# Kernel optimization log

Hardware: AMD Instinct MI355X
Metric: run time of the kernel (lower is better)

## Reference

```python
import jax, jax.numpy as jnp
import numpy as np

D_MODEL = 1024
N_HEADS = 16
SEQ = 512  # == max_seq_len; rel-pos bias requires n_token == max_seq_len


def setup_inputs() -> dict:
    key = jax.random.key(0)
    ks = jax.random.split(key, 12)
    B = 16
    x = jax.random.normal(ks[0], (B, SEQ, D_MODEL), dtype=jnp.float32)
    c = jax.random.normal(ks[1], (B, SEQ, 8), dtype=jnp.float32)  # unused by forward
    s = 1.0 / np.sqrt(D_MODEL)
    Wq = jax.random.normal(ks[2], (D_MODEL, D_MODEL), dtype=jnp.float32) * s
    bq = jnp.zeros((D_MODEL,), dtype=jnp.float32)
    Wk = jax.random.normal(ks[3], (D_MODEL, D_MODEL), dtype=jnp.float32) * s
    bk = jnp.zeros((D_MODEL,), dtype=jnp.float32)
    Wv = jax.random.normal(ks[4], (D_MODEL, D_MODEL), dtype=jnp.float32) * s
    bv = jnp.zeros((D_MODEL,), dtype=jnp.float32)
    Wo = jax.random.normal(ks[5], (D_MODEL, D_MODEL), dtype=jnp.float32) * s
    bo = jnp.zeros((D_MODEL,), dtype=jnp.float32)
    # trunc_normal_(std=0.02) approximated by normal*0.02 (values stay small)
    rel_table = jax.random.normal(ks[6], (2 * SEQ - 1, N_HEADS), dtype=jnp.float32) * 0.02
    return {"x": x, "c": c, "Wq": Wq, "bq": bq, "Wk": Wk, "bk": bk,
            "Wv": Wv, "bv": bv, "Wo": Wo, "bo": bo, "rel_table": rel_table}


def reference(x, c, Wq, bq, Wk, bk, Wv, bv, Wo, bo, rel_table):
    # x: [B, S, D]; c is unused in the original forward
    B, S, D = x.shape
    H = N_HEADS
    dk = D // H
    scale = 1.0 / np.sqrt(dk)

    q = (x @ Wq + bq).reshape(B, S, H, dk)
    k = (x @ Wk + bk).reshape(B, S, H, dk)
    v = (x @ Wv + bv).reshape(B, S, H, dk)

    # scores: [B, H, S, S]
    scores = jnp.einsum('bihd,bjhd->bhij', q, k) * scale

    # relative position bias: index[i,j] = i + (S-1-j), values in [0, 2S-2]
    rel_index = jnp.arange(S)[:, None] + jnp.arange(S - 1, -1, -1)[None, :]  # [S,S]
    bias = rel_table[rel_index]            # [S, S, H]
    scores = scores + jnp.transpose(bias, (2, 0, 1))[None]  # [1,H,S,S]

    # causal_mask=False: original adds False * -1e9 == 0, so no mask term
    probs = jax.nn.softmax(scores, axis=-1)

    out = jnp.einsum('bhij,bjhd->bihd', probs, v).reshape(B, S, D)
    return out @ Wo + bo
```

## Files before the change

kernel.cpp:

```cpp
#include <hip/hip_runtime.h>
#include <hip/hip_bf16.h>
#include <stdint.h>

#define D_MODEL 1024
#define NH 16
#define SEQ 512
#define DK 64
#define BATCH 16
#define M_TOT (BATCH*SEQ)

typedef unsigned short u16;
typedef unsigned int u32;
typedef __attribute__((ext_vector_type(8))) __bf16 bf16x8;
typedef __attribute__((ext_vector_type(4))) u16 ushort4v;
typedef __attribute__((ext_vector_type(4))) float f32x4;

static __device__ __forceinline__ u16 f2bf(float f) {
    union { float f; u32 i; } c; c.f = f;
    return (u16)((c.i + 0x8000u) >> 16);
}
static __device__ __forceinline__ u32 cvtpk(float lo, float hi) {
    u32 r; asm("v_cvt_pk_bf16_f32 %0, %1, %2" : "=v"(r) : "v"(lo), "v"(hi)); return r;
}
static __device__ __forceinline__ void async_copy16(const void* g, void* l) {
    __builtin_amdgcn_global_load_lds(
        (const __attribute__((address_space(1))) u32*)g,
        (__attribute__((address_space(3))) u32*)l, 16, 0, 0);
}
static __device__ __forceinline__ float fexp2(float x) {
    float r; asm("v_exp_f32 %0, %1" : "=v"(r) : "v"(x)); return r;
}

__global__ __launch_bounds__(256) void prep(const float* __restrict__ x,
                                            u16* __restrict__ xbf,
                                            const float* __restrict__ Wq,
                                            const float* __restrict__ Wk,
                                            const float* __restrict__ Wv,
                                            u16* __restrict__ Wt3) {
    __shared__ u16 tile[64][65];
    const int bid = blockIdx.x;
    const int t = threadIdx.x;
    if (bid < 2048) {
        #pragma unroll
        for (int it = 0; it < 4; ++it) {
            const int i = (bid * 1024 + it * 256 + t) * 4;
            float4 v = *(const float4*)&x[i];
            ushort4v o;
            o[0] = f2bf(v.x); o[1] = f2bf(v.y); o[2] = f2bf(v.z); o[3] = f2bf(v.w);
            *(ushort4v*)&xbf[i] = o;
        }
        return;
    }
    const int tw = bid - 2048;
    const int z = tw >> 8;
    const float* W = (z == 0) ? Wq : (z == 1) ? Wk : Wv;
    const int n0 = (tw & 15) * 64, k0 = ((tw >> 4) & 15) * 64;
    #pragma unroll
    for (int p = 0; p < 16; ++p) {
        int idx = p * 256 + t;
        int r = idx >> 6, c = idx & 63;
        tile[r][c] = f2bf(W[(size_t)(k0 + r) * D_MODEL + (n0 + c)]);
    }
    __syncthreads();
    #pragma unroll
    for (int p = 0; p < 16; ++p) {
        int idx = p * 256 + t;
        int r = idx >> 6, c = idx & 63;
        Wt3[((size_t)z * D_MODEL + n0 + r) * D_MODEL + (k0 + c)] = tile[c][r];
    }
}

__global__ __launch_bounds__(256) void gemm_bt(const u16* __restrict__ A,
                                               const u16* __restrict__ Bt,
                                               const float* __restrict__ b0,
                                               const float* __restrict__ b1,
                                               const float* __restrict__ b2,
                                               void* __restrict__ o0,
                                               void* __restrict__ o1,
                                               void* __restrict__ o2,
                                               int qkv) {
    __shared__ __attribute__((aligned(16))) u16 smem[16896];
    u16* Asm = smem;
    u16* Bsm = smem + 8192;
    const int t = threadIdx.x;
    const int m0 = blockIdx.y * 128, n0 = blockIdx.x * 128;
    const int lane = t & 63, w = t >> 6;
    const int lm = lane & 15, quad = lane >> 4;
    const int wm = w >> 1, wn = w & 1;

    f32x4 acc[4][4];
    #pragma unroll
    for (int i = 0; i < 4; ++i)
        #pragma unroll
        for (int j = 0; j < 4; ++j) acc[i][j] = (f32x4){0.f, 0.f, 0.f, 0.f};

    for (int kt = 0; kt < D_MODEL / 64; ++kt) {
        const int k0 = kt * 64;
        __syncthreads();
        #pragma unroll
        for (int i = 0; i < 4; ++i) {
            int chunk = i * 256 + t;
            int row = chunk >> 3, c = chunk & 7;
            int cs = c ^ (row & 7);
            async_copy16(A + (size_t)(m0 + row) * D_MODEL + k0 + cs * 8, &Asm[chunk * 8]);
        }
        #pragma unroll
        for (int i = 0; i < 4; ++i) {
            int chunk = i * 256 + t;
            int row = chunk >> 3, c = chunk & 7;
            int cs = c ^ (row & 7);
            async_copy16(Bt + (size_t)(n0 + row) * D_MODEL + k0 + cs * 8, &Bsm[chunk * 8]);
        }
        __syncthreads();
        #pragma unroll
        for (int ks = 0; ks < 64; ks += 32) {
            const int cbase = ks >> 3;
            bf16x8 af[4], bfv[4];
            #pragma unroll
            for (int im = 0; im < 4; ++im) {
                const int row = wm * 64 + im * 16 + lm;
                const int c = (cbase + quad) ^ (row & 7);
                af[im] = *(const bf16x8*)&Asm[row * 64 + c * 8];
            }
            #pragma unroll
            for (int in = 0; in < 4; ++in) {
                const int row = wn * 64 + in * 16 + lm;
                const int c = (cbase + quad) ^ (row & 7);
                bfv[in] = *(const bf16x8*)&Bsm[row * 64 + c * 8];
            }
            #pragma unroll
            for (int im = 0; im < 4; ++im)
                #pragma unroll
                for (int in = 0; in < 4; ++in)
                    acc[im][in] = __builtin_amdgcn_mfma_f32_16x16x32_bf16(
                        af[im], bfv[in], acc[im][in], 0, 0, 0);
        }
    }

    __syncthreads();
    if (qkv) {
        const int sel = n0 >> 10;
        if (sel == 2) {
            #pragma unroll
            for (int in = 0; in < 4; ++in) {
                const int nn = (n0 & 1023) + wn * 64 + in * 16 + lm;
                const float bv = b2[nn];
                const int h = nn >> 6, d = nn & 63;
                #pragma unroll
                for (int im = 0; im < 4; ++im) {
                    const int mb = m0 + wm * 64 + im * 16 + quad * 4;
                    const int b = mb >> 9, s = mb & 511;
                    ushort4v pk;
                    #pragma unroll
                    for (int r = 0; r < 4; ++r) pk[r] = f2bf(acc[im][in][r] + bv);
                    *(ushort4v*)&((u16*)o2)[((size_t)(b * NH + h) * DK + d) * SEQ + s] = pk;
                }
            }
        } else {
            u16* dst = sel ? (u16*)o1 : (u16*)o0;
            const float* bb = sel ? b1 : b0;
            u16 (*Cs)[132] = (u16(*)[132])smem;
            #pragma unroll
            for (int in = 0; in < 4; ++in) {
                const int nl = wn * 64 + in * 16 + lm;
                const float bv = bb[(n0 & 1023) + nl];
                #pragma unroll
                for (int im = 0; im < 4; ++im)
                    #pragma unroll
                    for (int r = 0; r < 4; ++r)
                        Cs[wm * 64 + im * 16 + quad * 4 + r][nl] =
                            f2bf(acc[im][in][r] + bv);
            }
            __syncthreads();
            const int rr = t >> 1, hh = t & 1;
            const int m = m0 + rr;
            const int b = m >> 9, s = m & 511;
            const int h = ((n0 & 1023) >> 6) + hh;
            u16* dp = &dst[((size_t)(b * NH + h) * SEQ + s) * DK];
            #pragma unroll
            for (int c = 0; c < 8; ++c)
                *(uint4*)&dp[c * 8] = *(const uint4*)&Cs[rr][hh * 64 + c * 8];
        }
    } else {
        float (*Cs)[132] = (float(*)[132])smem;
        #pragma unroll
        for (int ph = 0; ph < 2; ++ph) {
            if (wm == ph) {
                #pragma unroll
                for (int in = 0; in < 4; ++in) {
                    const int nl = wn * 64 + in * 16 + lm;
                    const float bv = b0[n0 + nl];
                    #pragma unroll
                    for (int im = 0; im < 4; ++im)
                        #pragma unroll
                        for (int r = 0; r < 4; ++r)
                            Cs[im * 16 + quad * 4 + r][nl] = acc[im][in][r] + bv;
                }
            }
            __syncthreads();
            const int rr = t >> 2, qq = t & 3;
            float* dp = &((float*)o0)[(size_t)(m0 + ph * 64 + rr) * D_MODEL + n0 + qq * 32];
            #pragma unroll
            for (int c = 0; c < 8; ++c)
                *(uint4*)&dp[c * 4] = *(const uint4*)&Cs[rr][qq * 32 + c * 4];
            __syncthreads();
        }
    }
}

__global__ __launch_bounds__(256) void attn_flash(const u16* __restrict__ qg,
                                                  const u16* __restrict__ kg,
                                                  const u16* __restrict__ vTg,
                                                  const float* __restrict__ rel,
                                                  u16* __restrict__ aout,
                                                  const float* __restrict__ Wo,
                                                  u16* __restrict__ WtO) {
    __shared__ __attribute__((aligned(16))) char smem_raw[53760];
    u16* ktb = (u16*)smem_raw;
    u16* vtb = (u16*)(smem_raw + 16384);
    float* biasb = (float*)(smem_raw + 32768);
    u16* qt = (u16*)(smem_raw + 35328);
    u16 (*Pl)[32][72] = (u16(*)[32][72])(smem_raw + 35328);

    const int t = threadIdx.x;
    const int F = blockIdx.x;
    if (F >= 1024) {
        u16 (*tile)[65] = (u16(*)[65])smem_raw;
        const int tw = F - 1024;
        const int n0 = (tw & 15) * 64, k0 = (tw >> 4) * 64;
        #pragma unroll
        for (int p = 0; p < 16; ++p) {
            int idx = p * 256 + t;
            int r = idx >> 6, c = idx & 63;
            tile[r][c] = f2bf(Wo[(size_t)(k0 + r) * D_MODEL + (n0 + c)]);
        }
        __syncthreads();
        #pragma unroll
        for (int p = 0; p < 16; ++p) {
            int idx = p * 256 + t;
            int r = idx >> 6, c = idx & 63;
            WtO[(size_t)(n0 + r) * D_MODEL + (k0 + c)] = tile[c][r];
        }
        return;
    }

    const int lane = t & 63, w = t >> 6;
    const int lm = lane & 15, quad = lane >> 4;
    const int xcd = F & 7, qti = (F >> 3) & 3, grp = F >> 5;
    const int p = grp * 8 + xcd;
    const int h = p & 15, b = p >> 4;
    const int q0 = qti * 128;
    const size_t bh = (size_t)(b * NH + h);
    const u16* qb = qg + bh * SEQ * DK;
    const u16* kb = kg + bh * SEQ * DK;
    const u16* vb = vTg + bh * DK * SEQ;

    #pragma unroll
    for (int i = 0; i < 2; ++i) {
        const int chunk = i * 256 + t, row = chunk >> 3, c = chunk & 7;
        const int cs = c ^ (row & 7);
        async_copy16(kb + row * DK + cs * 8, &ktb[chunk * 8]);
        async_copy16(vb + row * SEQ + cs * 8, &vtb[chunk * 8]);
    }

    #pragma unroll
    for (int i = 0; i < 4; ++i) {
        const int chunk = i * 256 + t, row = chunk >> 3, c = chunk & 7;
        const int cs = c ^ (row & 7);
        *(uint4*)&qt[chunk * 8] = *(const uint4*)&qb[(q0 + row) * DK + cs * 8];
    }
    for (int u = t; u < 639; u += 256) biasb[u] = rel[(q0 + u) * NH + h] * 1.44269504f;

    __syncthreads();

    bf16x8 aq[2][2];
    #pragma unroll
    for (int g = 0; g < 2; ++g) {
        const int ra = w * 32 + g * 16 + lm;
        aq[g][0] = *(const bf16x8*)&qt[ra * 64 + ((quad) ^ (ra & 7)) * 8];
        aq[g][1] = *(const bf16x8*)&qt[ra * 64 + ((4 + quad) ^ (ra & 7)) * 8];
    }
    __syncthreads();

    bf16x8 ones;
    #pragma unroll
    for (int i = 0; i < 8; ++i) ones[i] = (__bf16)1.0f;

    f32x4 ol[2];
    f32x4 o[2][4];
    #pragma unroll
    for (int g = 0; g < 2; ++g) {
        ol[g] = (f32x4){0.f, 0.f, 0.f, 0.f};
        #pragma unroll
        for (int sd = 0; sd < 4; ++sd) o[g][sd] = (f32x4){0.f, 0.f, 0.f, 0.f};
    }

    const float scale2 = 0.125f * 1.44269504f;

    for (int jt = 0; jt < 8; ++jt) {
        if (jt) __syncthreads();
        const int cur = jt & 1, nxt = cur ^ 1;
        u16* ktc = ktb + cur * 4096;
        u16* vtc = vtb + cur * 4096;
        if (jt < 7) {
            const int j1 = (jt + 1) * 64;
            u16* ktn = ktb + nxt * 4096;
            u16* vtn = vtb + nxt * 4096;
            #pragma unroll
            for (int i = 0; i < 2; ++i) {
                const int chunk = i * 256 + t, row = chunk >> 3, c = chunk & 7;
                const int cs = c ^ (row & 7);
                async_copy16(kb + (j1 + row) * DK + cs * 8, &ktn[chunk * 8]);
                async_copy16(vb + row * SEQ + j1 + cs * 8, &vtn[chunk * 8]);
            }
        }
        const int j0 = jt * 64;

        #pragma unroll
        for (int js = 0; js < 4; ++js) {
            const int rb = js * 16 + lm;
            bf16x8 bk0 = *(const bf16x8*)&ktc[rb * 64 + ((quad) ^ (rb & 7)) * 8];
            bf16x8 bk1 = *(const bf16x8*)&ktc[rb * 64 + ((4 + quad) ^ (rb & 7)) * 8];
            #pragma unroll
            for (int g = 0; g < 2; ++g) {
                f32x4 c = (f32x4){0.f, 0.f, 0.f, 0.f};
                c = __builtin_amdgcn_mfma_f32_16x16x32_bf16(bk0, aq[g][0], c, 0, 0, 0);
                c = __builtin_amdgcn_mfma_f32_16x16x32_bf16(bk1, aq[g][1], c, 0, 0, 0);
                const int bb0 = w * 32 + g * 16 + lm + 511 - j0 - js * 16 - quad * 4;
                float e0 = fexp2(c[0] * scale2 + biasb[bb0]);
                float e1 = fexp2(c[1] * scale2 + biasb[bb0 - 1]);
                float e2 = fexp2(c[2] * scale2 + biasb[bb0 - 2]);
                float e3 = fexp2(c[3] * scale2 + biasb[bb0 - 3]);
                uint2 pk = {cvtpk(e0, e1), cvtpk(e2, e3)};
                *(uint2*)&Pl[w][g * 16 + lm][js * 16 + quad * 4] = pk;
            }
        }

        bf16x8 ap[2][2];
        #pragma unroll
        for (int g = 0; g < 2; ++g) {
            ap[g][0] = *(const bf16x8*)&Pl[w][g * 16 + lm][quad * 8];
            ap[g][1] = *(const bf16x8*)&Pl[w][g * 16 + lm][32 + quad * 8];
            ol[g] = __builtin_amdgcn_mfma_f32_16x16x32_bf16(ones, ap[g][0], ol[g], 0, 0, 0);
            ol[g] = __builtin_amdgcn_mfma_f32_16x16x32_bf16(ones, ap[g][1], ol[g], 0, 0, 0);
        }
        #pragma unroll
        for (int sd = 0; sd < 4; ++sd) {
            const int rv = sd * 16 + lm;
            bf16x8 bv0 = *(const bf16x8*)&vtc[rv * 64 + ((quad) ^ (rv & 7)) * 8];
            bf16x8 bv1 = *(const bf16x8*)&vtc[rv * 64 + ((4 + quad) ^ (rv & 7)) * 8];
            #pragma unroll
            for (int g = 0; g < 2; ++g) {
                o[g][sd] = __builtin_amdgcn_mfma_f32_16x16x32_bf16(bv0, ap[g][0], o[g][sd], 0, 0, 0);
                o[g][sd] = __builtin_amdgcn_mfma_f32_16x16x32_bf16(bv1, ap[g][1], o[g][sd], 0, 0, 0);
            }
        }
    }

    #pragma unroll
    for (int g = 0; g < 2; ++g) {
        const float rinv = 1.0f / ol[g][0];
        #pragma unroll
        for (int sd = 0; sd < 4; ++sd) {
            uint2 pk = {cvtpk(o[g][sd][0] * rinv, o[g][sd][1] * rinv),
                        cvtpk(o[g][sd][2] * rinv, o[g][sd][3] * rinv)};
            *(uint2*)&Pl[w][g * 16 + lm][sd * 16 + quad * 4] = pk;
        }
    }
    const int rowl = lane >> 1, ch = lane & 1;
    u16* dp = aout + (size_t)(b * SEQ + q0 + w * 32 + rowl) * D_MODEL + h * DK + ch * 32;
    #pragma unroll
    for (int c = 0; c < 4; ++c)
        *(uint4*)&dp[c * 8] = *(const uint4*)&Pl[w][rowl][ch * 32 + c * 8];
}

extern "C" void kernel_launch(void* const* d_in, const int* in_sizes, int n_in,
                              void* d_out, int out_size, void* d_ws, size_t ws_size,
                              hipStream_t stream) {
    const float* x   = (const float*)d_in[0];
    const float* Wq  = (const float*)d_in[2];
    const float* bq  = (const float*)d_in[3];
    const float* Wk  = (const float*)d_in[4];
    const float* bk  = (const float*)d_in[5];
    const float* Wv  = (const float*)d_in[6];
    const float* bv  = (const float*)d_in[7];
    const float* Wo  = (const float*)d_in[8];
    const float* bo  = (const float*)d_in[9];
    const float* rel = (const float*)d_in[10];
    float* out = (float*)d_out;

    u16* ws = (u16*)d_ws;
    const size_t WSZ = (size_t)D_MODEL * D_MODEL;
    const size_t TSZ = (size_t)M_TOT * D_MODEL;
    u16* Wt3 = ws;
    u16* xbf = Wt3 + 3 * WSZ;
    u16* qws = xbf + TSZ;
    u16* kws = qws + TSZ;
    u16* vws = kws + TSZ;
    u16* aws = xbf;

    dim3 tb(256);
    prep<<<dim3(2048 + 768), tb, 0, stream>>>(x, xbf, Wq, Wk, Wv, Wt3);
    gemm_bt<<<dim3(24, 64), tb, 0, stream>>>(xbf, Wt3, bq, bk, bv, qws, kws, vws, 1);
    attn_flash<<<dim3(1024 + 256), tb, 0, stream>>>(qws, kws, vws, rel, aws, Wo, Wt3);
    gemm_bt<<<dim3(8, 64), tb, 0, stream>>>(aws, Wt3, bo, nullptr, nullptr,
                                            (void*)out, nullptr, nullptr, 0);
}
```

Baseline: 245.8 us.

## Add 256x256 8-wave pipelined QKV GEMM kernel with double-buffered async loads

Replaces the 128x128 QKV projection GEMM with a dedicated 512-thread kernel that computes 256x256 tiles. It double-buffers async global-to-LDS copies interleaved across eight sub-phases, raises MFMA priority with setprio, and remaps block indices for better L2 locality. The aim is more data reuse per tile and memory latency hidden behind MFMA work in the largest GEMM. The cost is 128KB of LDS per block, high register pressure from 32 accumulator tiles, and intricate vmcnt/barrier bookkeeping that could stall if the waits are mistuned.

Measured after the change: 254.8 us. 1.04x slower.

```diff
diff --git a/kernel.cpp b/kernel.cpp
--- a/kernel.cpp
+++ b/kernel.cpp
@@ -70,15 +70,155 @@
     }
 }
 
+__global__ __launch_bounds__(512, 2) void gemm_qkv8(const u16* __restrict__ A,
+                                                    const u16* __restrict__ Bt,
+                                                    const float* __restrict__ b0,
+                                                    const float* __restrict__ b1,
+                                                    const float* __restrict__ b2,
+                                                    u16* __restrict__ o0,
+                                                    u16* __restrict__ o1,
+                                                    u16* __restrict__ o2) {
+    __shared__ __attribute__((aligned(16))) u16 smem[65536];
+    const int t = threadIdx.x;
+    const int lin = blockIdx.y * 12 + blockIdx.x;
+    const int swz = (lin & 7) * 48 + (lin >> 3);
+    const int bx = swz % 12, by = swz / 12;
+    const int m0 = by * 256, n0 = bx * 256;
+    const int lane = t & 63, w = t >> 6;
+    const int lm = lane & 15, quad = lane >> 4;
+    const int wm2 = w >> 2, wn4 = w & 3;
+
+    f32x4 acc[8][4];
+    #pragma unroll
+    for (int i = 0; i < 8; ++i)
+        #pragma unroll
+        for (int j = 0; j < 4; ++j) acc[i][j] = (f32x4){0.f, 0.f, 0.f, 0.f};
+
+    auto stage = [&](int type , int half, int kt, int d) {
+        u16* dst = smem + d * 32768 + type * 16384 + half * 8192;
+        const u16* base = (type == 0) ? A + (size_t)(m0 + half * 128) * D_MODEL
+                                      : Bt + (size_t)(n0 + half * 128) * D_MODEL;
+        #pragma unroll
+        for (int i = 0; i < 2; ++i) {
+            const int idx = i * 512 + t;
+            const int row = idx >> 3, c = idx & 7;
+            const int cs = c ^ (row & 7);
+            async_copy16(base + (size_t)row * D_MODEL + kt * 64 + cs * 8, &dst[idx * 8]);
+        }
+    };
+
+    stage(0, 0, 0, 0); stage(0, 1, 0, 0); stage(1, 0, 0, 0); stage(1, 1, 0, 0);
+    stage(0, 0, 1, 1); stage(1, 0, 1, 1);
+    asm volatile("s_waitcnt vmcnt(4)" ::: "memory");
+    __builtin_amdgcn_s_barrier();
+
+    for (int it = 0; it < 8; ++it) {
+        const int k1 = 2 * it + 1, k2 = 2 * it + 2, k3 = 2 * it + 3;
+        bf16x8 bfr[2][2];
+        #pragma unroll
+        for (int p = 0; p < 8; ++p) {
+            const int d = p >> 2;
+            const int q = p & 3, mh = q & 1, nh = q >> 1;
+            const u16* As = smem + d * 32768 + mh * 8192;
+            const u16* Bs = smem + d * 32768 + 16384 + nh * 8192;
+            bf16x8 a[4][2];
+            #pragma unroll
+            for (int mf = 0; mf < 4; ++mf) {
+                const int rl = wm2 * 64 + mf * 16 + lm;
+                #pragma unroll
+                for (int ks = 0; ks < 2; ++ks)
+                    a[mf][ks] = *(const bf16x8*)&As[rl * 64 + ((ks * 4 + quad) ^ (rl & 7)) * 8];
+            }
+            if (mh == 0) {
+                #pragma unroll
+                for (int nf = 0; nf < 2; ++nf) {
+                    const int rl = wn4 * 32 + nf * 16 + lm;
+                    #pragma unroll
+                    for (int ks = 0; ks < 2; ++ks)
+                        bfr[nf][ks] = *(const bf16x8*)&Bs[rl * 64 + ((ks * 4 + quad) ^ (rl & 7)) * 8];
+                }
+            }
+            if (p == 0)      stage(0, 1, k1, 1);
+            else if (p == 1) stage(1, 1, k1, 1);
+            else if (p == 3) { if (it < 7) { stage(0, 0, k2, 0); stage(1, 0, k2, 0); } }
+            else if (p == 4) { if (it < 7) stage(0, 1, k2, 0); }
+            else if (p == 5) { if (it < 7) stage(1, 1, k2, 0); }
+            else if (p == 7) { if (it < 7) { stage(0, 0, k3, 1); stage(1, 0, k3, 1); } }
+            __builtin_amdgcn_s_barrier();
+            __builtin_amdgcn_s_setprio(1);
+            #pragma unroll
+            for (int ks = 0; ks < 2; ++ks)
+                #pragma unroll
+                for (int mf = 0; mf < 4; ++mf)
+                    #pragma unroll
+                    for (int nf = 0; nf < 2; ++nf)
+                        acc[mh * 4 + mf][nh * 2 + nf] = __builtin_amdgcn_mfma_f32_16x16x32_bf16(
+                            a[mf][ks], bfr[nf][ks], acc[mh * 4 + mf][nh * 2 + nf], 0, 0, 0);
+            __builtin_amdgcn_s_setprio(0);
+            if (p == 3) {
+                if (it < 7) { asm volatile("s_waitcnt vmcnt(4)" ::: "memory"); }
+                else        { asm volatile("s_waitcnt vmcnt(0)" ::: "memory"); }
+            }
+            if (p == 7 && it < 7) { asm volatile("s_waitcnt vmcnt(4)" ::: "memory"); }
+            __builtin_amdgcn_s_barrier();
+        }
+    }
+
+    __syncthreads();
+    const int sel = n0 >> 10;
+    if (sel == 2) {
+        #pragma unroll
+        for (int j = 0; j < 4; ++j) {
+            const int nn = (n0 & 1023) + (j >> 1) * 128 + wn4 * 32 + (j & 1) * 16 + lm;
+            const float bv = b2[nn];
+            const int h = nn >> 6, dd = nn & 63;
+            #pragma unroll
+            for (int i = 0; i < 8; ++i) {
+                const int mb = m0 + (i >> 2) * 128 + wm2 * 64 + (i & 3) * 16 + quad * 4;
+                const int bb_ = mb >> 9, s = mb & 511;
+                ushort4v pk;
+                #pragma unroll
+                for (int r = 0; r < 4; ++r) pk[r] = f2bf(acc[i][j][r] + bv);
+                *(ushort4v*)&o2[((size_t)(bb_ * NH + h) * DK + dd) * SEQ + s] = pk;
+            }
+        }
+    } else {
+        u16* dst = sel ? o1 : o0;
+        const float* bb = sel ? b1 : b0;
+        u16 (*Cs)[132] = (u16(*)[132])smem;
+        #pragma unroll
+        for (int ch = 0; ch < 2; ++ch) {
+            #pragma unroll
+            for (int jj = 0; jj < 2; ++jj) {
+                const int j = ch * 2 + jj;
+                const int nl = wn4 * 32 + jj * 16 + lm;
+                const float bv = bb[(n0 & 1023) + ch * 128 + nl];
+                #pragma unroll
+                for (int i = 0; i < 8; ++i) {
+                    const int row = (i >> 2) * 128 + wm2 * 64 + (i & 3) * 16 + quad * 4;
+                    #pragma unroll
+                    for (int r = 0; r < 4; ++r)
+                        Cs[row + r][nl] = f2bf(acc[i][j][r] + bv);
+                }
+            }
+            __syncthreads();
+            const int rr = t >> 1, hh = t & 1;
+            const int m = m0 + rr;
+            const int bb_ = m >> 9, s = m & 511;
+            const int h = (((n0 & 1023) + ch * 128) >> 6) + hh;
+            u16* dp = &dst[((size_t)(bb_ * NH + h) * SEQ + s) * DK];
+            #pragma unroll
+            for (int c = 0; c < 8; ++c)
+                *(uint4*)&dp[c * 8] = *(const uint4*)&Cs[rr][hh * 64 + c * 8];
+            __syncthreads();
+        }
+    }
+}
+
 __global__ __launch_bounds__(256) void gemm_bt(const u16* __restrict__ A,
                                                const u16* __restrict__ Bt,
                                                const float* __restrict__ b0,
-                                               const float* __restrict__ b1,
-                                               const float* __restrict__ b2,
-                                               void* __restrict__ o0,
-                                               void* __restrict__ o1,
-                                               void* __restrict__ o2,
-                                               int qkv) {
+                                               void* __restrict__ o0) {
     __shared__ __attribute__((aligned(16))) u16 smem[16896];
     u16* Asm = smem;
     u16* Bsm = smem + 8192;
@@ -138,73 +278,28 @@
     }
 
     __syncthreads();
-    if (qkv) {
-        const int sel = n0 >> 10;
-        if (sel == 2) {
-            #pragma unroll
-            for (int in = 0; in < 4; ++in) {
-                const int nn = (n0 & 1023) + wn * 64 + in * 16 + lm;
-                const float bv = b2[nn];
-                const int h = nn >> 6, d = nn & 63;
-                #pragma unroll
-                for (int im = 0; im < 4; ++im) {
-                    const int mb = m0 + wm * 64 + im * 16 + quad * 4;
-                    const int b = mb >> 9, s = mb & 511;
-                    ushort4v pk;
-                    #pragma unroll
-                    for (int r = 0; r < 4; ++r) pk[r] = f2bf(acc[im][in][r] + bv);
-                    *(ushort4v*)&((u16*)o2)[((size_t)(b * NH + h) * DK + d) * SEQ + s] = pk;
-                }
-            }
-        } else {
-            u16* dst = sel ? (u16*)o1 : (u16*)o0;
-            const float* bb = sel ? b1 : b0;
-            u16 (*Cs)[132] = (u16(*)[132])smem;
+    float (*Cs)[132] = (float(*)[132])smem;
+    #pragma unroll
+    for (int ph = 0; ph < 2; ++ph) {
+        if (wm == ph) {
             #pragma unroll
             for (int in = 0; in < 4; ++in) {
                 const int nl = wn * 64 + in * 16 + lm;
-                const float bv = bb[(n0 & 1023) + nl];
+                const float bv = b0[n0 + nl];
                 #pragma unroll
                 for (int im = 0; im < 4; ++im)
                     #pragma unroll
                     for (int r = 0; r < 4; ++r)
-                        Cs[wm * 64 + im * 16 + quad * 4 + r][nl] =
-                            f2bf(acc[im][in][r] + bv);
-            }
-            __syncthreads();
-            const int rr = t >> 1, hh = t & 1;
-            const int m = m0 + rr;
-            const int b = m >> 9, s = m & 511;
-            const int h = ((n0 & 1023) >> 6) + hh;
-            u16* dp = &dst[((size_t)(b * NH + h) * SEQ + s) * DK];
-            #pragma unroll
-            for (int c = 0; c < 8; ++c)
-                *(uint4*)&dp[c * 8] = *(const uint4*)&Cs[rr][hh * 64 + c * 8];
-        }
-    } else {
-        float (*Cs)[132] = (float(*)[132])smem;
-        #pragma unroll
-        for (int ph = 0; ph < 2; ++ph) {
-            if (wm == ph) {
-                #pragma unroll
-                for (int in = 0; in < 4; ++in) {
-                    const int nl = wn * 64 + in * 16 + lm;
-                    const float bv = b0[n0 + nl];
-                    #pragma unroll
-                    for (int im = 0; im < 4; ++im)
-                        #pragma unroll
-                        for (int r = 0; r < 4; ++r)
-                            Cs[im * 16 + quad * 4 + r][nl] = acc[im][in][r] + bv;
-                }
-            }
-            __syncthreads();
-            const int rr = t >> 2, qq = t & 3;
-            float* dp = &((float*)o0)[(size_t)(m0 + ph * 64 + rr) * D_MODEL + n0 + qq * 32];
-            #pragma unroll
-            for (int c = 0; c < 8; ++c)
-                *(uint4*)&dp[c * 4] = *(const uint4*)&Cs[rr][qq * 32 + c * 4];
-            __syncthreads();
-        }
+                        Cs[im * 16 + quad * 4 + r][nl] = acc[im][in][r] + bv;
+            }
+        }
+        __syncthreads();
+        const int rr = t >> 2, qq = t & 3;
+        float* dp = &((float*)o0)[(size_t)(m0 + ph * 64 + rr) * D_MODEL + n0 + qq * 32];
+        #pragma unroll
+        for (int c = 0; c < 8; ++c)
+            *(uint4*)&dp[c * 4] = *(const uint4*)&Cs[rr][qq * 32 + c * 4];
+        __syncthreads();
     }
 }
 
@@ -401,8 +496,7 @@
 
     dim3 tb(256);
     prep<<<dim3(2048 + 768), tb, 0, stream>>>(x, xbf, Wq, Wk, Wv, Wt3);
-    gemm_bt<<<dim3(24, 64), tb, 0, stream>>>(xbf, Wt3, bq, bk, bv, qws, kws, vws, 1);
+    gemm_qkv8<<<dim3(12, 32), dim3(512), 0, stream>>>(xbf, Wt3, bq, bk, bv, qws, kws, vws);
     attn_flash<<<dim3(1024 + 256), tb, 0, stream>>>(qws, kws, vws, rel, aws, Wo, Wt3);
-    gemm_bt<<<dim3(8, 64), tb, 0, stream>>>(aws, Wt3, bo, nullptr, nullptr,
-                                            (void*)out, nullptr, nullptr, 0);
-}
+    gemm_bt<<<dim3(8, 64), tb, 0, stream>>>(aws, Wt3, bo, (void*)out);
+}
```
